# Performance work log

Hardware: AMD Instinct MI355X
Metric: run time of the kernel (lower is better)

The kernel has to match this reference:

```python
import jax, jax.numpy as jnp
import numpy as np

B, S, HIDDEN = 2, 2048, 2048
HQ, HKV, D = 16, 4, 128
EPS = 1e-6
SCALE = D ** -0.5


def _deinterleave(x):
    # [..., D] interleaved pairs -> [x0,x2,...,x1,x3,...] (half layout)
    *lead, d = x.shape
    return x.reshape(*lead, d // 2, 2).swapaxes(-1, -2).reshape(*lead, d)


def _interleave(x):
    # inverse of _deinterleave
    *lead, d = x.shape
    return x.reshape(*lead, 2, d // 2).swapaxes(-1, -2).reshape(*lead, d)


def _rotate_half(x):
    x1, x2 = jnp.split(x, 2, axis=-1)
    return jnp.concatenate([-x2, x1], axis=-1)


def _rmsnorm(x, w):
    var = jnp.mean(jnp.square(x), axis=-1, keepdims=True)
    return x * jax.lax.rsqrt(var + EPS) * w


def setup_inputs() -> dict:
    key = jax.random.key(0)
    k0, k1, k2, k3, k4 = jax.random.split(key, 5)
    hidden_states = jax.random.normal(k0, (B, S, HIDDEN), jnp.float32)
    cos = jax.random.uniform(k1, (S, D), jnp.float32, -1.0, 1.0)
    sin = jax.random.uniform(k2, (S, D), jnp.float32, -1.0, 1.0)
    qkv_w = jax.random.normal(k3, ((HQ + 2 * HKV) * D, HIDDEN), jnp.float32) * 0.02
    qk_norm_w = jnp.ones((D,), jnp.float32)
    o_w = jax.random.normal(k4, (HIDDEN, HQ * D), jnp.float32) * 0.02
    return {"hidden_states": hidden_states, "cos": cos, "sin": sin,
            "qkv_w": qkv_w, "qk_norm_w": qk_norm_w, "o_w": o_w}


def reference(hidden_states, cos, sin, qkv_w, qk_norm_w, o_w):
    b, s, _ = hidden_states.shape
    qkv = jnp.einsum('bsh,oh->bso', hidden_states, qkv_w)  # [B,S,(HQ+2HKV)*D]
    q = qkv[..., : HQ * D].reshape(b, s, HQ, D)
    k = qkv[..., HQ * D:(HQ + HKV) * D].reshape(b, s, HKV, D)
    v = qkv[..., (HQ + HKV) * D:].reshape(b, s, HKV, D)

    # interleaved-layout RoPE: deinterleave -> rotate-half RoPE -> re-interleave
    q, k = _deinterleave(q), _deinterleave(k)
    cs = cos[None, :, None, :]
    sn = sin[None, :, None, :]
    q = q * cs + _rotate_half(q) * sn
    k = k * cs + _rotate_half(k) * sn
    q, k = _interleave(q), _interleave(k)

    # QK RMSNorm (shared weight over head_dim)
    q = _rmsnorm(q, qk_norm_w)
    k = _rmsnorm(k, qk_norm_w)

    # causal GQA attention
    g = HQ // HKV
    qg = q.reshape(b, s, HKV, g, D)
    scores = jnp.einsum('bshgd,bthd->bhgst', qg, k) * SCALE  # [B,HKV,g,S,S]
    causal = jnp.tril(jnp.ones((s, s), bool))
    scores = jnp.where(causal, scores, jnp.finfo(scores.dtype).min)
    probs = jax.nn.softmax(scores, axis=-1)
    attn = jnp.einsum('bhgst,bthd->bshgd', probs, v).reshape(b, s, HQ * D)

    return jnp.einsum('bsd,od->bso', attn, o_w)
```

## Files before the change

kernel.cpp:

```cpp
#include <hip/hip_runtime.h>
#include <hip/hip_bf16.h>

typedef __bf16 bf16_t;
typedef bf16_t bf16x8 __attribute__((ext_vector_type(8)));
typedef float f32x4 __attribute__((ext_vector_type(4)));
typedef float f32x16 __attribute__((ext_vector_type(16)));
typedef unsigned short u16;
typedef unsigned int u32;

#define B_    2
#define S_    2048
#define HID   2048
#define NQKV  3072
#define HQ_   16
#define HKV_  4
#define D_    128
#define QSCALE_ 0.12751879526600565f

__device__ __forceinline__ u16 f2b(float f) {
    __hip_bfloat16 h = __float2bfloat16(f);
    return *reinterpret_cast<u16*>(&h);
}

__global__ __launch_bounds__(256) void cvt_f32_bf16(const float* __restrict__ in,
                                                    u16* __restrict__ out, int n4) {
    int i = blockIdx.x * 256 + threadIdx.x;
    if (i >= n4) return;
    float4 v = reinterpret_cast<const float4*>(in)[i];
    ushort4 o;
    o.x = f2b(v.x); o.y = f2b(v.y); o.z = f2b(v.z); o.w = f2b(v.w);
    reinterpret_cast<ushort4*>(out)[i] = o;
}

__global__ __launch_bounds__(256) void gemm_bt_bf16(const u16* __restrict__ A,
                                                    const u16* __restrict__ Bm,
                                                    float* __restrict__ C,
                                                    int M, int N, int K) {
    __shared__ u16 As[128 * 32];
    __shared__ u16 Bs[128 * 32];
    const int tid  = threadIdx.x;
    const int lane = tid & 63;
    const int wave = tid >> 6;
    const int wr = wave >> 1, wc = wave & 1;
    const int lrow = lane & 15, lgrp = lane >> 4;
    const int m0 = blockIdx.x * 128;
    const int n0 = blockIdx.y * 128;

    const int c0 = tid, c1 = tid + 256;
    const u16* aG0 = A  + (size_t)(m0 + (c0 >> 2)) * K + (c0 & 3) * 8;
    const u16* aG1 = A  + (size_t)(m0 + (c1 >> 2)) * K + (c1 & 3) * 8;
    const u16* bG0 = Bm + (size_t)(n0 + (c0 >> 2)) * K + (c0 & 3) * 8;
    const u16* bG1 = Bm + (size_t)(n0 + (c1 >> 2)) * K + (c1 & 3) * 8;

    f32x4 acc[4][4] = {};

    for (int k0 = 0; k0 < K; k0 += 32) {
        __builtin_amdgcn_global_load_lds(
            (const __attribute__((address_space(1))) void*)(aG0 + k0),
            (__attribute__((address_space(3))) void*)(As + c0 * 8), 16, 0, 0);
        __builtin_amdgcn_global_load_lds(
            (const __attribute__((address_space(1))) void*)(aG1 + k0),
            (__attribute__((address_space(3))) void*)(As + c1 * 8), 16, 0, 0);
        __builtin_amdgcn_global_load_lds(
            (const __attribute__((address_space(1))) void*)(bG0 + k0),
            (__attribute__((address_space(3))) void*)(Bs + c0 * 8), 16, 0, 0);
        __builtin_amdgcn_global_load_lds(
            (const __attribute__((address_space(1))) void*)(bG1 + k0),
            (__attribute__((address_space(3))) void*)(Bs + c1 * 8), 16, 0, 0);
        __syncthreads();

        bf16x8 af[4], bfr[4];
        #pragma unroll
        for (int mi = 0; mi < 4; mi++)
            af[mi] = *(const bf16x8*)(As + (wr * 64 + mi * 16 + lrow) * 32 + lgrp * 8);
        #pragma unroll
        for (int ni = 0; ni < 4; ni++)
            bfr[ni] = *(const bf16x8*)(Bs + (wc * 64 + ni * 16 + lrow) * 32 + lgrp * 8);
        #pragma unroll
        for (int mi = 0; mi < 4; mi++)
            #pragma unroll
            for (int ni = 0; ni < 4; ni++)
                acc[mi][ni] = __builtin_amdgcn_mfma_f32_16x16x32_bf16(
                    af[mi], bfr[ni], acc[mi][ni], 0, 0, 0);
        __syncthreads();
    }

    #pragma unroll
    for (int mi = 0; mi < 4; mi++) {
        #pragma unroll
        for (int ni = 0; ni < 4; ni++) {
            #pragma unroll
            for (int i = 0; i < 4; i++) {
                int r = m0 + wr * 64 + mi * 16 + lgrp * 4 + i;
                int c = n0 + wc * 64 + ni * 16 + lrow;
                C[(size_t)r * N + c] = acc[mi][ni][i];
            }
        }
    }
}

__global__ __launch_bounds__(256) void rope_norm_split(const float* __restrict__ qkv,
                                                       const float* __restrict__ cosb,
                                                       const float* __restrict__ sinb,
                                                       const float* __restrict__ nw,
                                                       u16* __restrict__ qb,
                                                       u16* __restrict__ kb,
                                                       u16* __restrict__ vb) {
    const int row  = blockIdx.x;
    const int b    = row >> 11;
    const int s    = row & 2047;
    const int wave = threadIdx.x >> 6;
    const int lane = threadIdx.x & 63;
    const float* base = qkv + (size_t)row * NQKV;

    const float c0 = cosb[s * 128 + lane];
    const float c1 = cosb[s * 128 + 64 + lane];
    const float s0 = sinb[s * 128 + lane];
    const float s1 = sinb[s * 128 + 64 + lane];
    const float w0 = nw[2 * lane];
    const float w1 = nw[2 * lane + 1];

    for (int h = wave; h < HQ_ + HKV_; h += 4) {
        float2 x = *(const float2*)(base + h * 128 + 2 * lane);
        float y0 = x.x * c0 - x.y * s0;
        float y1 = x.y * c1 + x.x * s1;
        float ss = y0 * y0 + y1 * y1;
        #pragma unroll
        for (int off = 32; off; off >>= 1) ss += __shfl_xor(ss, off);
        float r = rsqrtf(ss * (1.0f / 128.0f) + 1e-6f);
        float o0 = y0 * r * w0, o1 = y1 * r * w1;
        if (h < HQ_) {
            u32 pack = (u32)f2b(o0 * QSCALE_) | ((u32)f2b(o1 * QSCALE_) << 16);
            *(u32*)(qb + ((size_t)(b * HQ_ + h) * S_ + s) * D_ + 2 * lane) = pack;
        } else {
            u32 pack = (u32)f2b(o0) | ((u32)f2b(o1) << 16);
            *(u32*)(kb + ((size_t)(b * HKV_ + (h - HQ_)) * S_ + s) * D_ + 2 * lane) = pack;
        }
    }
    {
        int h = wave;
        float2 x = *(const float2*)(base + (HQ_ + HKV_) * 128 + h * 128 + 2 * lane);
        u32 pack = (u32)f2b(x.x) | ((u32)f2b(x.y) << 16);
        *(u32*)(vb + ((size_t)(b * HKV_ + h) * S_ + s) * D_ + 2 * lane) = pack;
    }
}

__global__ __launch_bounds__(256) void transpose_v(const u16* __restrict__ vb,
                                                   u16* __restrict__ vtb) {
    __shared__ u16 t[64][72];
    const int s0 = blockIdx.x * 64, d0 = blockIdx.y * 64, bh = blockIdx.z;
    const u16* src = vb  + (size_t)bh * S_ * D_;
    u16*       dst = vtb + (size_t)bh * D_ * S_;
    const int tid = threadIdx.x;

    {
        int r = tid >> 3, c8 = (tid & 7) * 8;
        #pragma unroll
        for (int p = 0; p < 2; p++) {
            int rr = r + p * 32;
            *(uint4*)&t[rr][c8] = *(const uint4*)(src + (size_t)(s0 + rr) * D_ + d0 + c8);
        }
    }
    __syncthreads();
    {
        int dd = tid & 63;
        int sb = (tid >> 6) * 8;
        #pragma unroll
        for (int p = 0; p < 2; p++) {
            int ss8 = sb + p * 32;
            union { u16 u[8]; uint4 v; } pk;
            #pragma unroll
            for (int j = 0; j < 8; j++) pk.u[j] = t[ss8 + j][dd];
            *(uint4*)(dst + (size_t)(d0 + dd) * S_ + s0 + ss8) = pk.v;
        }
    }
}

__global__ __launch_bounds__(256, 2) void attn_fwd3(const u16* __restrict__ qb,
                                                    const u16* __restrict__ kb,
                                                    const u16* __restrict__ vtb,
                                                    u16* __restrict__ attn) {
    __shared__ __align__(16) u16 Ks[2][64 * 128];
    __shared__ __align__(16) u16 Vs[2][128 * 64];

    const int bh  = blockIdx.y;
    const int qt  = (bh < 16) ? (15 - (int)blockIdx.x) : (int)blockIdx.x;
    const int b   = bh >> 4, hq = bh & 15, hkv = hq >> 2;
    const int tid = threadIdx.x;
    const int wave = tid >> 6, lane = tid & 63;
    const int l31 = lane & 31, hi = lane >> 5;
    const int swz = (l31 & 7) << 4;

    const u16* Q  = qb  + (size_t)(b * HQ_  + hq ) * S_ * D_;
    const u16* Kp = kb  + (size_t)(b * HKV_ + hkv) * S_ * D_;
    const u16* Vt = vtb + (size_t)(b * HKV_ + hkv) * D_ * S_;
    const int q0w = qt * 128 + wave * 32;
    const int qg  = q0w + l31;

    int kSrc[4], vSrc[4], cLds[4];
    #pragma unroll
    for (int p = 0; p < 4; p++) {
        int c = tid + p * 256;
        int kr = c >> 4, kc = ((c & 15) * 16) ^ ((kr & 7) << 4);
        kSrc[p] = kr * D_ + (kc >> 1);
        int vr = c >> 3, vc = ((c & 7) * 16) ^ ((vr & 7) << 4);
        vSrc[p] = vr * S_ + (vc >> 1);
        cLds[p] = c * 16;
    }

    auto STAGE = [&](int buf, int kv0s) {
        const u16* kbase = Kp + (size_t)kv0s * D_;
        const u16* vbase = Vt + kv0s;
        #pragma unroll
        for (int p = 0; p < 4; p++)
            __builtin_amdgcn_global_load_lds(
                (const __attribute__((address_space(1))) void*)(kbase + kSrc[p]),
                (__attribute__((address_space(3))) void*)((char*)Ks[buf] + cLds[p]), 16, 0, 0);
        #pragma unroll
        for (int p = 0; p < 4; p++)
            __builtin_amdgcn_global_load_lds(
                (const __attribute__((address_space(1))) void*)(vbase + vSrc[p]),
                (__attribute__((address_space(3))) void*)((char*)Vs[buf] + cLds[p]), 16, 0, 0);
    };

    bf16x8 qf[8];
    #pragma unroll
    for (int ds = 0; ds < 8; ds++)
        qf[ds] = *(const bf16x8*)(Q + (size_t)qg * D_ + ds * 16 + hi * 8);

    float m_run = -1e30f, l_run = 0.f;
    f32x16 oacc[4] = {};

    const int nkt = 2 * qt + 2;
    STAGE(0, 0);

    for (int kt = 0; kt < nkt; kt++) {
        const int cur = kt & 1;
        const int kv0 = kt * 64;
        if (kt + 1 < nkt) {
            STAGE(cur ^ 1, kv0 + 64);
            asm volatile("s_waitcnt vmcnt(8)" ::: "memory");
        } else {
            asm volatile("s_waitcnt vmcnt(0)" ::: "memory");
        }
        __builtin_amdgcn_s_barrier();

        const char* ksb = (const char*)Ks[cur];
        f32x16 sc[2] = {};
        __builtin_amdgcn_s_setprio(1);
        #pragma unroll
        for (int blk = 0; blk < 2; blk++) {
            const char* rowb = ksb + (blk * 32 + l31) * 256;
            #pragma unroll
            for (int ds = 0; ds < 8; ds++) {
                bf16x8 kf = *(const bf16x8*)(rowb + ((ds * 32 + hi * 16) ^ swz));
                sc[blk] = __builtin_amdgcn_mfma_f32_32x32x16_bf16(kf, qf[ds], sc[blk], 0, 0, 0);
            }
        }
        __builtin_amdgcn_s_setprio(0);

        if (kv0 + 63 > q0w) {
            #pragma unroll
            for (int blk = 0; blk < 2; blk++)
                #pragma unroll
                for (int r = 0; r < 16; r++) {
                    int kvg = kv0 + blk * 32 + (r & 3) + 8 * (r >> 2) + 4 * hi;
                    if (kvg > qg) sc[blk][r] = -1e30f;
                }
        }

        float t16[16];
        #pragma unroll
        for (int r = 0; r < 16; r++) t16[r] = fmaxf(sc[0][r], sc[1][r]);
        #pragma unroll
        for (int r = 0; r < 8; r++) t16[r] = fmaxf(t16[r], t16[r + 8]);
        #pragma unroll
        for (int r = 0; r < 4; r++) t16[r] = fmaxf(t16[r], t16[r + 4]);
        float mt = fmaxf(fmaxf(t16[0], t16[1]), fmaxf(t16[2], t16[3]));
        mt = fmaxf(mt, __shfl_xor(mt, 32));

        bool noDefer = !__all(mt <= m_run + 8.0f);
        float mnew = m_run;
        if (noDefer) {
            mnew = fmaxf(m_run, mt);
            float alpha = __builtin_amdgcn_exp2f(m_run - mnew);
            l_run *= alpha;
            #pragma unroll
            for (int d4 = 0; d4 < 4; d4++)
                #pragma unroll
                for (int r = 0; r < 16; r++) oacc[d4][r] *= alpha;
            m_run = mnew;
        }

        float la = 0.f;
        u32 pk0[8], pk1[8];
        #pragma unroll
        for (int g = 0; g < 4; g++)
            #pragma unroll
            for (int e = 0; e < 2; e++) {
                float a0 = __builtin_amdgcn_exp2f(sc[0][g * 4 + 2 * e]     - mnew);
                float b0 = __builtin_amdgcn_exp2f(sc[0][g * 4 + 2 * e + 1] - mnew);
                float a1 = __builtin_amdgcn_exp2f(sc[1][g * 4 + 2 * e]     - mnew);
                float b1 = __builtin_amdgcn_exp2f(sc[1][g * 4 + 2 * e + 1] - mnew);
                la += (a0 + b0) + (a1 + b1);
                pk0[g * 2 + e] = (u32)f2b(a0) | ((u32)f2b(b0) << 16);
                pk1[g * 2 + e] = (u32)f2b(a1) | ((u32)f2b(b1) << 16);
            }
        la += __shfl_xor(la, 32);
        l_run += la;

        u32 qk0[8], qk1[8];
        #pragma unroll
        for (int i = 0; i < 8; i++) {
            qk0[i] = __shfl_xor(pk0[i], 32);
            qk1[i] = __shfl_xor(pk1[i], 32);
        }

        const char* vsb = (const char*)Vs[cur];
        #pragma unroll
        for (int ks = 0; ks < 4; ks++) {
            const int i0 = (ks & 1) * 4;
            union { u32 w[4]; bf16x8 v; } pf;
            if (ks & 2) {
                pf.w[0] = hi ? qk1[i0 + 2] : pk1[i0 + 0];
                pf.w[1] = hi ? qk1[i0 + 3] : pk1[i0 + 1];
                pf.w[2] = hi ? pk1[i0 + 2] : qk1[i0 + 0];
                pf.w[3] = hi ? pk1[i0 + 3] : qk1[i0 + 1];
            } else {
                pf.w[0] = hi ? qk0[i0 + 2] : pk0[i0 + 0];
                pf.w[1] = hi ? qk0[i0 + 3] : pk0[i0 + 1];
                pf.w[2] = hi ? pk0[i0 + 2] : qk0[i0 + 0];
                pf.w[3] = hi ? pk0[i0 + 3] : qk0[i0 + 1];
            }
            __builtin_amdgcn_s_setprio(1);
            #pragma unroll
            for (int d4 = 0; d4 < 4; d4++) {
                bf16x8 vf = *(const bf16x8*)(vsb + (d4 * 32 + l31) * 128
                                                 + ((ks * 32 + hi * 16) ^ swz));
                oacc[d4] = __builtin_amdgcn_mfma_f32_32x32x16_bf16(vf, pf.v, oacc[d4], 0, 0, 0);
            }
            __builtin_amdgcn_s_setprio(0);
        }
        __builtin_amdgcn_s_barrier();
    }

    const float inv = 1.0f / l_run;
    u16* sl = (u16*)Ks + wave * (32 * 128);
    #pragma unroll
    for (int d4 = 0; d4 < 4; d4++)
        #pragma unroll
        for (int rp = 0; rp < 8; rp++) {
            int dbyte = d4 * 64 + 16 * (rp >> 1) + 8 * hi + 4 * (rp & 1);
            u32 w = (u32)f2b(oacc[d4][rp * 2] * inv)
                  | ((u32)f2b(oacc[d4][rp * 2 + 1] * inv) << 16);
            *(u32*)((char*)sl + l31 * 256 + (dbyte ^ swz)) = w;
        }
    #pragma unroll
    for (int j = 0; j < 8; j++) {
        int c = lane + j * 64;
        int qL = c >> 4, dc = c & 15;
        uint4 v = *(uint4*)((char*)sl + qL * 256 + ((dc * 16) ^ ((qL & 7) << 4)));
        int qrow = qt * 128 + wave * 32 + qL;
        *(uint4*)(attn + (size_t)(b * S_ + qrow) * (HQ_ * D_) + hq * D_ + dc * 8) = v;
    }
}

extern "C" void kernel_launch(void* const* d_in, const int* in_sizes, int n_in,
                              void* d_out, int out_size, void* d_ws, size_t ws_size,
                              hipStream_t stream) {
    const float* hidden = (const float*)d_in[0];
    const float* cosb   = (const float*)d_in[1];
    const float* sinb   = (const float*)d_in[2];
    const float* qkvw   = (const float*)d_in[3];
    const float* nw     = (const float*)d_in[4];
    const float* ow     = (const float*)d_in[5];
    float* out = (float*)d_out;

    const size_t M  = (size_t)B_ * S_;
    char* ws = (char*)d_ws;
    size_t off = 0;
    u16*   hb    = (u16*)(ws + off); off += M * HID * 2;
    u16*   wqkvb = (u16*)(ws + off); off += (size_t)NQKV * HID * 2;
    u16*   wob   = (u16*)(ws + off); off += (size_t)HID * (HQ_ * D_) * 2;
    float* qkv   = (float*)(ws + off); off += M * NQKV * 4;
    u16*   qb2   = (u16*)(ws + off); off += (size_t)B_ * HQ_  * S_ * D_ * 2;
    u16*   kb2   = (u16*)(ws + off); off += (size_t)B_ * HKV_ * S_ * D_ * 2;
    u16*   vb2   = (u16*)(ws + off); off += (size_t)B_ * HKV_ * S_ * D_ * 2;
    u16*   vtb   = (u16*)(ws + off); off += (size_t)B_ * HKV_ * S_ * D_ * 2;
    u16*   attn  = hb;

    {
        int n4 = (int)(M * HID / 4);
        cvt_f32_bf16<<<(n4 + 255) / 256, 256, 0, stream>>>(hidden, hb, n4);
    }
    {
        int n4 = NQKV * HID / 4;
        cvt_f32_bf16<<<(n4 + 255) / 256, 256, 0, stream>>>(qkvw, wqkvb, n4);
    }
    {
        int n4 = HID * (HQ_ * D_) / 4;
        cvt_f32_bf16<<<(n4 + 255) / 256, 256, 0, stream>>>(ow, wob, n4);
    }

    gemm_bt_bf16<<<dim3(M / 128, NQKV / 128), 256, 0, stream>>>(hb, wqkvb, qkv,
                                                                (int)M, NQKV, HID);

    rope_norm_split<<<(int)M, 256, 0, stream>>>(qkv, cosb, sinb, nw, qb2, kb2, vb2);

    transpose_v<<<dim3(S_ / 64, D_ / 64, B_ * HKV_), 256, 0, stream>>>(vb2, vtb);

    attn_fwd3<<<dim3(16, B_ * HQ_), 256, 0, stream>>>(qb2, kb2, vtb, attn);

    gemm_bt_bf16<<<dim3(M / 128, HID / 128), 256, 0, stream>>>(attn, wob, out,
                                                               (int)M, HID, HQ_ * D_);
}
```

Before: 241.3 us.

## Replace GEMM with 256x256-tile double-buffered swizzled LDS pipeline

Both projection GEMMs now use a new 512-thread kernel with 256x256 output tiles, a K-step of 64 and double-buffered LDS staged via global_load_lds. The LDS layout is XOR-swizzled, and prefetch of the next tile is interleaved with MFMA phases, using wave priority and explicit vmcnt waits. The aim is more data reuse per load and hiding global latency behind compute. In exchange, grids shrink to 192 and 128 blocks, fewer than the number of CUs, and each block uses 128KB of LDS.

Measured after the change: 232.9 us. -3.5%, faster.

```diff
diff --git a/kernel.cpp b/kernel.cpp
--- a/kernel.cpp
+++ b/kernel.cpp
@@ -32,71 +32,147 @@
     reinterpret_cast<ushort4*>(out)[i] = o;
 }
 
-__global__ __launch_bounds__(256) void gemm_bt_bf16(const u16* __restrict__ A,
-                                                    const u16* __restrict__ Bm,
-                                                    float* __restrict__ C,
-                                                    int M, int N, int K) {
-    __shared__ u16 As[128 * 32];
-    __shared__ u16 Bs[128 * 32];
+__global__ __launch_bounds__(512, 1) void gemm256_bt(const u16* __restrict__ A,
+                                                     const u16* __restrict__ Bm,
+                                                     float* __restrict__ C,
+                                                     int M, int N, int K) {
+    extern __shared__ __align__(16) char smem[];
+    u16* Asm = (u16*)smem;
+    u16* Bsm = (u16*)smem + 32768;
+
     const int tid  = threadIdx.x;
     const int lane = tid & 63;
-    const int wave = tid >> 6;
-    const int wr = wave >> 1, wc = wave & 1;
+    const int wid  = tid >> 6;
+    const int wr = wid >> 2, wc = wid & 3;
     const int lrow = lane & 15, lgrp = lane >> 4;
-    const int m0 = blockIdx.x * 128;
-    const int n0 = blockIdx.y * 128;
-
-    const int c0 = tid, c1 = tid + 256;
-    const u16* aG0 = A  + (size_t)(m0 + (c0 >> 2)) * K + (c0 & 3) * 8;
-    const u16* aG1 = A  + (size_t)(m0 + (c1 >> 2)) * K + (c1 & 3) * 8;
-    const u16* bG0 = Bm + (size_t)(n0 + (c0 >> 2)) * K + (c0 & 3) * 8;
-    const u16* bG1 = Bm + (size_t)(n0 + (c1 >> 2)) * K + (c1 & 3) * 8;
-
-    f32x4 acc[4][4] = {};
-
-    for (int k0 = 0; k0 < K; k0 += 32) {
+    const int swz  = (lrow & 7) << 4;
+    const int m0 = blockIdx.x * 256, n0 = blockIdx.y * 256;
+
+    const int stRow = tid >> 3;
+    const int stCol = ((((tid & 7) * 16) ^ ((stRow & 7) << 4)) >> 1);
+
+    const u16* aBase = A  + (size_t)(m0 + stRow) * K + stCol;
+    const u16* bBase = Bm + (size_t)(n0 + stRow) * K + stCol;
+
+    auto glds = [&](const u16* g, u16* l) {
         __builtin_amdgcn_global_load_lds(
-            (const __attribute__((address_space(1))) void*)(aG0 + k0),
-            (__attribute__((address_space(3))) void*)(As + c0 * 8), 16, 0, 0);
-        __builtin_amdgcn_global_load_lds(
-            (const __attribute__((address_space(1))) void*)(aG1 + k0),
-            (__attribute__((address_space(3))) void*)(As + c1 * 8), 16, 0, 0);
-        __builtin_amdgcn_global_load_lds(
-            (const __attribute__((address_space(1))) void*)(bG0 + k0),
-            (__attribute__((address_space(3))) void*)(Bs + c0 * 8), 16, 0, 0);
-        __builtin_amdgcn_global_load_lds(
-            (const __attribute__((address_space(1))) void*)(bG1 + k0),
-            (__attribute__((address_space(3))) void*)(Bs + c1 * 8), 16, 0, 0);
-        __syncthreads();
-
-        bf16x8 af[4], bfr[4];
-        #pragma unroll
-        for (int mi = 0; mi < 4; mi++)
-            af[mi] = *(const bf16x8*)(As + (wr * 64 + mi * 16 + lrow) * 32 + lgrp * 8);
-        #pragma unroll
-        for (int ni = 0; ni < 4; ni++)
-            bfr[ni] = *(const bf16x8*)(Bs + (wc * 64 + ni * 16 + lrow) * 32 + lgrp * 8);
-        #pragma unroll
-        for (int mi = 0; mi < 4; mi++)
-            #pragma unroll
-            for (int ni = 0; ni < 4; ni++)
-                acc[mi][ni] = __builtin_amdgcn_mfma_f32_16x16x32_bf16(
-                    af[mi], bfr[ni], acc[mi][ni], 0, 0, 0);
-        __syncthreads();
+            (const __attribute__((address_space(1))) void*)g,
+            (__attribute__((address_space(3))) void*)l, 16, 0, 0);
+    };
+    auto stageA = [&](int buf, int h, int k0) {
+        const u16* g = aBase + (size_t)(128 * h) * K + k0;
+        u16* d = Asm + buf * 16384 + (1024 * h + tid) * 8;
+        glds(g, d);
+        glds(g + (size_t)64 * K, d + 512 * 8);
+    };
+    auto stageB = [&](int buf, int h, int k0) {
+        const u16* g = bBase + (size_t)(128 * h) * K + k0;
+        u16* d = Bsm + buf * 16384 + (1024 * h + tid) * 8;
+        glds(g, d);
+        glds(g + (size_t)64 * K, d + 512 * 8);
+    };
+
+    f32x4 acc[8][4] = {};
+    const int KT = K >> 6;
+
+    stageA(0, 0, 0); stageA(0, 1, 0); stageB(0, 0, 0); stageB(0, 1, 0);
+
+    for (int x = 0; x < KT; ++x) {
+        const int cur = x & 1;
+        const int kn  = (x + 1) << 6;
+        const bool pf = (x + 1 < KT);
+        const char* aT = (const char*)(Asm + cur * 16384);
+        const char* bT = (const char*)(Bsm + cur * 16384);
+
+        auto ldA = [&](int mi, int ks) -> bf16x8 {
+            int row = wr * 128 + mi * 16 + lrow;
+            return *(const bf16x8*)(aT + row * 128 + ((ks * 64 + lgrp * 16) ^ swz));
+        };
+        auto ldB = [&](int ni, int ks) -> bf16x8 {
+            int row = wc * 64 + ni * 16 + lrow;
+            return *(const bf16x8*)(bT + row * 128 + ((ks * 64 + lgrp * 16) ^ swz));
+        };
+
+        bf16x8 afr[4][2], bfr[2][2];
+
+        if (pf) {
+            stageA(cur ^ 1, 0, kn);
+            asm volatile("s_waitcnt vmcnt(2)" ::: "memory");
+        } else {
+            asm volatile("s_waitcnt vmcnt(0)" ::: "memory");
+        }
+        __builtin_amdgcn_s_barrier();
+        #pragma unroll
+        for (int mi = 0; mi < 4; ++mi) { afr[mi][0] = ldA(mi, 0); afr[mi][1] = ldA(mi, 1); }
+        #pragma unroll
+        for (int ni = 0; ni < 2; ++ni) { bfr[ni][0] = ldB(ni, 0); bfr[ni][1] = ldB(ni, 1); }
+        __builtin_amdgcn_s_setprio(1);
+        #pragma unroll
+        for (int mi = 0; mi < 4; ++mi)
+            #pragma unroll
+            for (int ni = 0; ni < 2; ++ni) {
+                acc[mi][ni] = __builtin_amdgcn_mfma_f32_16x16x32_bf16(afr[mi][0], bfr[ni][0], acc[mi][ni], 0, 0, 0);
+                acc[mi][ni] = __builtin_amdgcn_mfma_f32_16x16x32_bf16(afr[mi][1], bfr[ni][1], acc[mi][ni], 0, 0, 0);
+            }
+        __builtin_amdgcn_s_setprio(0);
+        __builtin_amdgcn_s_barrier();
+
+        #pragma unroll
+        for (int ni = 0; ni < 2; ++ni) { bfr[ni][0] = ldB(ni + 2, 0); bfr[ni][1] = ldB(ni + 2, 1); }
+        if (pf) stageA(cur ^ 1, 1, kn);
+        __builtin_amdgcn_s_barrier();
+        __builtin_amdgcn_s_setprio(1);
+        #pragma unroll
+        for (int mi = 0; mi < 4; ++mi)
+            #pragma unroll
+            for (int ni = 0; ni < 2; ++ni) {
+                acc[mi][ni + 2] = __builtin_amdgcn_mfma_f32_16x16x32_bf16(afr[mi][0], bfr[ni][0], acc[mi][ni + 2], 0, 0, 0);
+                acc[mi][ni + 2] = __builtin_amdgcn_mfma_f32_16x16x32_bf16(afr[mi][1], bfr[ni][1], acc[mi][ni + 2], 0, 0, 0);
+            }
+        __builtin_amdgcn_s_setprio(0);
+        __builtin_amdgcn_s_barrier();
+
+        #pragma unroll
+        for (int mi = 0; mi < 4; ++mi) { afr[mi][0] = ldA(mi + 4, 0); afr[mi][1] = ldA(mi + 4, 1); }
+        if (pf) stageB(cur ^ 1, 0, kn);
+        __builtin_amdgcn_s_barrier();
+        __builtin_amdgcn_s_setprio(1);
+        #pragma unroll
+        for (int mi = 0; mi < 4; ++mi)
+            #pragma unroll
+            for (int ni = 0; ni < 2; ++ni) {
+                acc[mi + 4][ni + 2] = __builtin_amdgcn_mfma_f32_16x16x32_bf16(afr[mi][0], bfr[ni][0], acc[mi + 4][ni + 2], 0, 0, 0);
+                acc[mi + 4][ni + 2] = __builtin_amdgcn_mfma_f32_16x16x32_bf16(afr[mi][1], bfr[ni][1], acc[mi + 4][ni + 2], 0, 0, 0);
+            }
+        __builtin_amdgcn_s_setprio(0);
+        __builtin_amdgcn_s_barrier();
+
+        #pragma unroll
+        for (int ni = 0; ni < 2; ++ni) { bfr[ni][0] = ldB(ni, 0); bfr[ni][1] = ldB(ni, 1); }
+        if (pf) stageB(cur ^ 1, 1, kn);
+        __builtin_amdgcn_s_barrier();
+        __builtin_amdgcn_s_setprio(1);
+        #pragma unroll
+        for (int mi = 0; mi < 4; ++mi)
+            #pragma unroll
+            for (int ni = 0; ni < 2; ++ni) {
+                acc[mi + 4][ni] = __builtin_amdgcn_mfma_f32_16x16x32_bf16(afr[mi][0], bfr[ni][0], acc[mi + 4][ni], 0, 0, 0);
+                acc[mi + 4][ni] = __builtin_amdgcn_mfma_f32_16x16x32_bf16(afr[mi][1], bfr[ni][1], acc[mi + 4][ni], 0, 0, 0);
+            }
+        __builtin_amdgcn_s_setprio(0);
+        __builtin_amdgcn_s_barrier();
     }
 
     #pragma unroll
-    for (int mi = 0; mi < 4; mi++) {
-        #pragma unroll
-        for (int ni = 0; ni < 4; ni++) {
-            #pragma unroll
-            for (int i = 0; i < 4; i++) {
-                int r = m0 + wr * 64 + mi * 16 + lgrp * 4 + i;
-                int c = n0 + wc * 64 + ni * 16 + lrow;
-                C[(size_t)r * N + c] = acc[mi][ni][i];
-            }
-        }
-    }
+    for (int mi = 0; mi < 8; ++mi)
+        #pragma unroll
+        for (int ni = 0; ni < 4; ++ni) {
+            int r = m0 + wr * 128 + mi * 16 + lgrp * 4;
+            int c = n0 + wc * 64 + ni * 16 + lrow;
+            float* p = C + (size_t)r * N + c;
+            #pragma unroll
+            for (int i = 0; i < 4; ++i) p[(size_t)i * N] = acc[mi][ni][i];
+        }
 }
 
 __global__ __launch_bounds__(256) void rope_norm_split(const float* __restrict__ qkv,
@@ -402,8 +478,12 @@
         cvt_f32_bf16<<<(n4 + 255) / 256, 256, 0, stream>>>(ow, wob, n4);
     }
 
-    gemm_bt_bf16<<<dim3(M / 128, NQKV / 128), 256, 0, stream>>>(hb, wqkvb, qkv,
-                                                                (int)M, NQKV, HID);
+    const int smemSz = 131072;
+    hipFuncSetAttribute(reinterpret_cast<const void*>(gemm256_bt),
+                        hipFuncAttributeMaxDynamicSharedMemorySize, smemSz);
+
+    gemm256_bt<<<dim3(M / 256, NQKV / 256), 512, smemSz, stream>>>(hb, wqkvb, qkv,
+                                                                   (int)M, NQKV, HID);
 
     rope_norm_split<<<(int)M, 256, 0, stream>>>(qkv, cosb, sinb, nw, qb2, kb2, vb2);
 
@@ -411,6 +491,6 @@
 
     attn_fwd3<<<dim3(16, B_ * HQ_), 256, 0, stream>>>(qb2, kb2, vtb, attn);
 
-    gemm_bt_bf16<<<dim3(M / 128, HID / 128), 256, 0, stream>>>(attn, wob, out,
-                                                               (int)M, HID, HQ_ * D_);
-}
+    gemm256_bt<<<dim3(M / 256, HID / 256), 512, smemSz, stream>>>(attn, wob, out,
+                                                                  (int)M, HID, HQ_ * D_);
+}
```
